# Optimization experiments

Hardware: AMD Instinct MI355X
Metric: run time of the kernel (lower is better)

The kernel has to match this reference:

```python
import jax, jax.numpy as jnp
import numpy as np

# ---- model constants (match init_kwargs) ----
NX, NY, H, K, GRID = 32, 1, 64, 3, 5
MID = 2 * H + 1            # 129, middle width of each KAN block
NB = GRID + K              # 8 B-spline basis functions per edge
BATCH = 65536


def _grid_pts():
    # uniform extended grid on [-1, 1] with K extra knots each side: GRID+2K+1 pts
    step = 2.0 / GRID
    return jnp.arange(-K, GRID + K + 1, dtype=jnp.float32) * step - 1.0


def bspline_basis(x):
    """Cox-de Boor B-spline bases. x: [B, I] -> [B, I, GRID+K]."""
    g = _grid_pts()[None, None, :]          # [1,1,P]
    xe = x[..., None]                       # [B,I,1]
    B0 = ((xe >= g[..., :-1]) & (xe < g[..., 1:])).astype(x.dtype)
    Bp = B0
    for p in range(1, K + 1):
        left = (xe - g[..., :-(p + 1)]) / (g[..., p:-1] - g[..., :-(p + 1)])
        right = (g[..., p + 1:] - xe) / (g[..., p + 1:] - g[..., 1:-p])
        Bp = left * Bp[..., :-1] + right * Bp[..., 1:]
    return Bp  # [B, I, NB]


def kan_layer(x, coef, sb, ss, bias):
    """pykan KANLayer: y_o = sum_i sb[i,o]*silu(x_i) + ss[i,o]*spline_io(x_i) + bias_o.
    x: [B,I]; coef: [I,O,NB]; sb, ss: [I,O]; bias: [O]."""
    bs = bspline_basis(x)                                   # [B,I,NB]
    spline = jnp.einsum('bip,iop->bo', bs, coef * ss[:, :, None])
    return jax.nn.silu(x) @ sb + spline + bias


def setup_inputs() -> dict:
    key = jax.random.key(0)
    ks = iter(jax.random.split(key, 40))

    def xavier(k, shape, fan_in, fan_out):
        gain = np.sqrt(2.0)  # relu gain, as in the torch module
        std = gain * np.sqrt(2.0 / (fan_in + fan_out))
        return (std * jax.random.normal(k, shape, dtype=jnp.float32))

    inp = {
        'x': jax.random.normal(next(ks), (BATCH, NX), dtype=jnp.float32),
        'W_in': xavier(next(ks), (NX, H), NX, H),
        'b_in': jnp.zeros((H,), jnp.float32),
        'W_out': xavier(next(ks), (H, NY), H, NY),
    }
    for l in range(2):  # num_hidden_layers KAN blocks, each = 2 KANLayers
        for tag, (din, dout) in [('a', (H, MID)), ('b', (MID, H))]:
            inp[f'coef{l}{tag}'] = xavier(next(ks), (din, dout, NB), din * NB, dout)
            inp[f'sb{l}{tag}'] = xavier(next(ks), (din, dout), din, dout)
            inp[f'ss{l}{tag}'] = jnp.ones((din, dout), jnp.float32)
            inp[f'bias{l}{tag}'] = jnp.zeros((dout,), jnp.float32)
    return inp


def reference(x, W_in, b_in, W_out,
              coef0a, sb0a, ss0a, bias0a, coef0b, sb0b, ss0b, bias0b,
              coef1a, sb1a, ss1a, bias1a, coef1b, sb1b, ss1b, bias1b):
    h = jax.nn.relu(x @ W_in + b_in)
    for (ca, sa, ta, ba, cb, sbb, tb, bb) in (
        (coef0a, sb0a, ss0a, bias0a, coef0b, sb0b, ss0b, bias0b),
        (coef1a, sb1a, ss1a, bias1a, coef1b, sb1b, ss1b, bias1b),
    ):
        h = kan_layer(h, ca, sa, ta, ba)   # H -> 2H+1
        h = kan_layer(h, cb, sbb, tb, bb)  # 2H+1 -> H
    return jax.nn.sigmoid(h @ W_out)       # [B, NY]
```

## Files before the change

kernel.cpp:

```cpp
#include <hip/hip_runtime.h>
#include <math.h>
#include <stdint.h>

#define BATCH 65536
#define TB 64

typedef __fp16   fp16x2 __attribute__((ext_vector_type(2)));
typedef _Float16 half8  __attribute__((ext_vector_type(8)));
typedef float   floatx4 __attribute__((ext_vector_type(4)));

#define SH 68
#define SM 130
#define HM_SLICE (16*SM + 64)

#define WIN 2048
#define KSA 18
#define KSB 39
#define WA (KSA*9*512)
#define WB (KSB*4*512)
#define WTOT (WIN + 2*(WA+WB))

__global__ void setup_weights(
    const float* __restrict__ W_in,
    const float* __restrict__ c0a, const float* __restrict__ sb0a, const float* __restrict__ ss0a,
    const float* __restrict__ c0b, const float* __restrict__ sb0b, const float* __restrict__ ss0b,
    const float* __restrict__ c1a, const float* __restrict__ sb1a, const float* __restrict__ ss1a,
    const float* __restrict__ c1b, const float* __restrict__ sb1b, const float* __restrict__ ss1b,
    _Float16* __restrict__ wt) {
  int idx = blockIdx.x * 256 + threadIdx.x;
  if (idx >= WTOT) return;
  float v = 0.0f;
  if (idx < WIN) {
    int nt = idx >> 9; int r = idx & 511; int l = r >> 3; int j = r & 7;
    int n = nt*16 + (l & 15);
    int k = (l >> 4)*8 + j;
    v = W_in[k*64 + n];
  } else {
    int e2   = idx - WIN;
    int pair = (e2 >= WA + WB) ? 1 : 0;
    int e    = e2 - pair * (WA + WB);
    if (e < WA) {
      const float* coef = pair ? c1a : c0a;
      const float* sb   = pair ? sb1a : sb0a;
      const float* ss   = pair ? ss1a : ss0a;
      int ks = e / 4608; int r = e - ks*4608;
      int nt = r >> 9;   int q = r & 511;
      int l  = q >> 3;   int j = q & 7;
      int n  = nt*16 + (l & 15);
      int k  = ks*32 + (l >> 4)*8 + j;
      if (n < 129) {
        if (k < 512) { int i = k >> 3, p = k & 7; v = ss[i*129+n] * coef[(i*129+n)*8 + p]; }
        else         { int i = k - 512;           v = sb[i*129+n]; }
      }
    } else {
      const float* coef = pair ? c1b : c0b;
      const float* sb   = pair ? sb1b : sb0b;
      const float* ss   = pair ? ss1b : ss0b;
      int eb = e - WA;
      int ks = eb >> 11; int r = eb & 2047;
      int nt = r >> 9;   int q = r & 511;
      int l  = q >> 3;   int j = q & 7;
      int n  = nt*16 + (l & 15);
      int k  = ks*32 + (l >> 4)*8 + j;
      if (k < 1088) { int i = k >> 3, p = k & 7; if (i < 129) v = ss[i*64+n] * coef[(i*64+n)*8 + p]; }
      else          { int i = k - 1088;          if (i < 129) v = sb[i*64+n]; }
    }
  }
  wt[idx] = (_Float16)v;
}

__device__ __forceinline__ half8 feat8(float x) {
  float s  = (x + 2.2f) * 2.5f;
  float mf = floorf(s);
  int   m  = (int)mf;
  float u  = s - mf;
  float t  = 1.0f - u;
  float u2 = u*u;
  float w0 = t*t*t * (1.0f/6.0f);
  float w3 = u2*u * (1.0f/6.0f);
  float w1 = fmaf(u2, fmaf(0.5f, u, -1.0f), 2.0f/3.0f);
  float w2 = 1.0f - w0 - w1 - w3;
  union { fp16x2 h2[2]; uint64_t u64; } P;
  P.h2[0] = __builtin_amdgcn_cvt_pkrtz(w0, w1);
  P.h2[1] = __builtin_amdgcn_cvt_pkrtz(w2, w3);
  uint64_t w01 = (m >= 0 && m <= 10) ? P.u64 : 0ull;
  int sh = (m - 3) * 16;
  uint64_t q0 = (sh >= 0) ? ((sh < 64) ? (w01 << sh) : 0ull) : (w01 >> (-sh));
  uint64_t q1 = (sh >= 64) ? (w01 << (sh - 64))
                           : ((sh > 0) ? (w01 >> (64 - sh)) : 0ull);
  union { uint64_t q[2]; half8 h; } R;
  R.q[0] = q0; R.q[1] = q1;
  return R.h;
}

template<int KSPL, int KSIL, int NT, int SIN, int O, int SOUT>
__device__ __forceinline__ void kan_layer(
    const _Float16* __restrict__ hinw, _Float16* __restrict__ houtw,
    const _Float16* __restrict__ wt, const float* __restrict__ bias, int lane) {
  constexpr int KTOT = KSPL + KSIL;
  constexpr int PF   = (NT > 4) ? 4 : NT;
  const int ln = lane & 15;
  const int kq = lane >> 4;
  const half8* __restrict__ bp = (const half8*)wt + lane;
  floatx4 acc[NT];
  #pragma unroll
  for (int j = 0; j < NT; ++j) acc[j] = (floatx4){0.f, 0.f, 0.f, 0.f};

  half8 Bpre[PF];
  #pragma unroll
  for (int j = 0; j < PF; ++j) Bpre[j] = bp[j*64];

  #pragma unroll 2
  for (int ks = 0; ks < KTOT; ++ks) {
    half8 A;
    if (ks < KSPL) {
      float xv = (float)hinw[ln*SIN + ks*4 + kq];
      A = feat8(xv);
    } else {
      int sk = ks - KSPL;
      half8 h8 = *(const half8*)&hinw[ln*SIN + sk*32 + kq*8];
      union { fp16x2 h2[4]; half8 v; } Au;
      #pragma unroll
      for (int e = 0; e < 4; ++e) {
        float x0 = (float)h8[2*e], x1 = (float)h8[2*e + 1];
        float s0 = x0 / (1.0f + __expf(-x0));
        float s1 = x1 / (1.0f + __expf(-x1));
        Au.h2[e] = __builtin_amdgcn_cvt_pkrtz(s0, s1);
      }
      A = Au.v;
    }
    half8 Bcur[PF];
    #pragma unroll
    for (int j = 0; j < PF; ++j) Bcur[j] = Bpre[j];
    const int nks = (ks + 1 < KTOT) ? (ks + 1) : ks;
    #pragma unroll
    for (int j = 0; j < PF; ++j) Bpre[j] = bp[(nks*NT + j)*64];
    #pragma unroll
    for (int j = 0; j < PF; ++j)
      acc[j] = __builtin_amdgcn_mfma_f32_16x16x32_f16(A, Bcur[j], acc[j], 0, 0, 0);
    #pragma unroll
    for (int j = PF; j < NT; ++j) {
      half8 B = bp[(ks*NT + j)*64];
      acc[j] = __builtin_amdgcn_mfma_f32_16x16x32_f16(A, B, acc[j], 0, 0, 0);
    }
  }

  #pragma unroll
  for (int j = 0; j < NT; ++j) {
    int col = j*16 + ln;
    if (col < O) {
      float bv = bias[col];
      #pragma unroll
      for (int r = 0; r < 4; ++r)
        houtw[(kq*4 + r)*SOUT + col] = (_Float16)(acc[j][r] + bv);
    }
  }
}

extern "C" __global__ void __launch_bounds__(256, 4)
kan_forward(const float* __restrict__ x, const float* __restrict__ b_in,
            const float* __restrict__ W_out, const _Float16* __restrict__ wt,
            const float* __restrict__ bias0a, const float* __restrict__ bias0b,
            const float* __restrict__ bias1a, const float* __restrict__ bias1b,
            float* __restrict__ out) {
  __shared__ _Float16 hM[4][HM_SLICE];
  __shared__ _Float16 hH[4][16*SH];
  const int t    = threadIdx.x;
  const int wv   = t >> 6;
  const int lane = t & 63;
  const int ln   = lane & 15;
  const int kq   = lane >> 4;
  _Float16* hMw = hM[wv];
  _Float16* hHw = hH[wv];
  const int rbase = blockIdx.x * TB + wv * 16;

  hMw[16*SM + lane] = (_Float16)0.0f;
  if (lane < 16) hMw[lane*SM + 129] = (_Float16)0.0f;

  {
    const float* xr = &x[(rbase + ln)*32 + kq*8];
    float4 v0 = *(const float4*)&xr[0];
    float4 v1 = *(const float4*)&xr[4];
    union { fp16x2 h2[4]; half8 h8; } A;
    A.h2[0] = __builtin_amdgcn_cvt_pkrtz(v0.x, v0.y);
    A.h2[1] = __builtin_amdgcn_cvt_pkrtz(v0.z, v0.w);
    A.h2[2] = __builtin_amdgcn_cvt_pkrtz(v1.x, v1.y);
    A.h2[3] = __builtin_amdgcn_cvt_pkrtz(v1.z, v1.w);
    const half8* bp = (const half8*)wt + lane;
    #pragma unroll
    for (int nt = 0; nt < 4; ++nt) {
      floatx4 z = (floatx4){0.f, 0.f, 0.f, 0.f};
      half8 B = bp[nt*64];
      floatx4 a = __builtin_amdgcn_mfma_f32_16x16x32_f16(A.h8, B, z, 0, 0, 0);
      int col = nt*16 + ln;
      float bv = b_in[col];
      #pragma unroll
      for (int r = 0; r < 4; ++r)
        hHw[(kq*4 + r)*SH + col] = (_Float16)fmaxf(a[r] + bv, 0.0f);
    }
  }

  kan_layer<16,2,9,SH,129,SM>(hHw, hMw, wt + WIN,             bias0a, lane);
  kan_layer<34,5,4,SM, 64,SH>(hMw, hHw, wt + WIN + WA,        bias0b, lane);
  kan_layer<16,2,9,SH,129,SM>(hHw, hMw, wt + WIN + WA + WB,   bias1a, lane);
  kan_layer<34,5,4,SM, 64,SH>(hMw, hHw, wt + WIN + 2*WA + WB, bias1b, lane);

  {
    float s = 0.0f;
    #pragma unroll
    for (int j = 0; j < 16; ++j)
      s = fmaf((float)hHw[ln*SH + kq*16 + j], W_out[kq*16 + j], s);
    s += __shfl_down(s, 32);
    s += __shfl_down(s, 16);
    if (lane < 16) out[rbase + ln] = 1.0f / (1.0f + __expf(-s));
  }
}

extern "C" void kernel_launch(void* const* d_in, const int* in_sizes, int n_in,
                              void* d_out, int out_size, void* d_ws, size_t ws_size,
                              hipStream_t stream) {
  const float* x     = (const float*)d_in[0];
  const float* W_in  = (const float*)d_in[1];
  const float* b_in  = (const float*)d_in[2];
  const float* W_out = (const float*)d_in[3];
  const float* c0a = (const float*)d_in[4];  const float* sb0a = (const float*)d_in[5];
  const float* ss0a= (const float*)d_in[6];  const float* bias0a=(const float*)d_in[7];
  const float* c0b = (const float*)d_in[8];  const float* sb0b = (const float*)d_in[9];
  const float* ss0b= (const float*)d_in[10]; const float* bias0b=(const float*)d_in[11];
  const float* c1a = (const float*)d_in[12]; const float* sb1a = (const float*)d_in[13];
  const float* ss1a= (const float*)d_in[14]; const float* bias1a=(const float*)d_in[15];
  const float* c1b = (const float*)d_in[16]; const float* sb1b = (const float*)d_in[17];
  const float* ss1b= (const float*)d_in[18]; const float* bias1b=(const float*)d_in[19];
  float*    out = (float*)d_out;
  _Float16* wt  = (_Float16*)d_ws;

  setup_weights<<<(WTOT + 255)/256, 256, 0, stream>>>(
      W_in, c0a, sb0a, ss0a, c0b, sb0b, ss0b,
      c1a, sb1a, ss1a, c1b, sb1b, ss1b, wt);

  kan_forward<<<BATCH/TB, 256, 0, stream>>>(
      x, b_in, W_out, wt, bias0a, bias0b, bias1a, bias1b, out);
}
```

Before: 176.7 us.

## Switch KAN layers to 32x32x16 MFMA with 32-row wave tiles

Each wave now handles 32 batch rows and uses the 32x32x16 f16 MFMA instead of 16x16x32. The packed weight layout is rebuilt for the new tile shape, and the B-operand prefetch becomes a two-stage full-width double buffer. The aim is to reuse each weight fragment across twice as many rows and cut weight-load traffic per row. In exchange, accumulators and shared memory per wave grow and occupancy is lowered to 2 blocks per SM. The layer-b spline K range is also tightened from 1088 to 1040, which removes some padded k-steps.

```diff
diff --git a/kernel.cpp b/kernel.cpp
--- a/kernel.cpp
+++ b/kernel.cpp
@@ -3,21 +3,21 @@
 #include <stdint.h>
 
 #define BATCH 65536
-#define TB 64
-
-typedef __fp16   fp16x2 __attribute__((ext_vector_type(2)));
-typedef _Float16 half8  __attribute__((ext_vector_type(8)));
-typedef float   floatx4 __attribute__((ext_vector_type(4)));
+#define TB 128
+
+typedef __fp16   fp16x2  __attribute__((ext_vector_type(2)));
+typedef _Float16 half8   __attribute__((ext_vector_type(8)));
+typedef float    floatx16 __attribute__((ext_vector_type(16)));
 
 #define SH 68
 #define SM 130
-#define HM_SLICE (16*SM + 64)
+#define HM_SLICE (32*SM + 64)
 
 #define WIN 2048
-#define KSA 18
-#define KSB 39
-#define WA (KSA*9*512)
-#define WB (KSB*4*512)
+#define KSA 36
+#define KSB 74
+#define WA (KSA*5*512)
+#define WB (KSB*2*512)
 #define WTOT (WIN + 2*(WA+WB))
 
 __global__ void setup_weights(
@@ -31,9 +31,10 @@
   if (idx >= WTOT) return;
   float v = 0.0f;
   if (idx < WIN) {
-    int nt = idx >> 9; int r = idx & 511; int l = r >> 3; int j = r & 7;
-    int n = nt*16 + (l & 15);
-    int k = (l >> 4)*8 + j;
+    int ks = idx >> 10; int nt = (idx >> 9) & 1;
+    int q = idx & 511;  int l = q >> 3;   int j = q & 7;
+    int n = nt*32 + (l & 31);
+    int k = ks*16 + (l >> 5)*8 + j;
     v = W_in[k*64 + n];
   } else {
     int e2   = idx - WIN;
@@ -43,11 +44,11 @@
       const float* coef = pair ? c1a : c0a;
       const float* sb   = pair ? sb1a : sb0a;
       const float* ss   = pair ? ss1a : ss0a;
-      int ks = e / 4608; int r = e - ks*4608;
+      int ks = e / 2560; int r = e - ks*2560;
       int nt = r >> 9;   int q = r & 511;
       int l  = q >> 3;   int j = q & 7;
-      int n  = nt*16 + (l & 15);
-      int k  = ks*32 + (l >> 4)*8 + j;
+      int n  = nt*32 + (l & 31);
+      int k  = ks*16 + (l >> 5)*8 + j;
       if (n < 129) {
         if (k < 512) { int i = k >> 3, p = k & 7; v = ss[i*129+n] * coef[(i*129+n)*8 + p]; }
         else         { int i = k - 512;           v = sb[i*129+n]; }
@@ -57,13 +58,13 @@
       const float* sb   = pair ? sb1b : sb0b;
       const float* ss   = pair ? ss1b : ss0b;
       int eb = e - WA;
-      int ks = eb >> 11; int r = eb & 2047;
+      int ks = eb >> 10; int r = eb & 1023;
       int nt = r >> 9;   int q = r & 511;
       int l  = q >> 3;   int j = q & 7;
-      int n  = nt*16 + (l & 15);
-      int k  = ks*32 + (l >> 4)*8 + j;
-      if (k < 1088) { int i = k >> 3, p = k & 7; if (i < 129) v = ss[i*64+n] * coef[(i*64+n)*8 + p]; }
-      else          { int i = k - 1088;          if (i < 129) v = sb[i*64+n]; }
+      int n  = nt*32 + (l & 31);
+      int k  = ks*16 + (l >> 5)*8 + j;
+      if (k < 1032)      { int i = k >> 3, p = k & 7; v = ss[i*64+n] * coef[(i*64+n)*8 + p]; }
+      else if (k >= 1040){ int s = k - 1040; if (s < 129) v = sb[s*64+n]; }
     }
   }
   wt[idx] = (_Float16)v;
@@ -98,27 +99,30 @@
     const _Float16* __restrict__ hinw, _Float16* __restrict__ houtw,
     const _Float16* __restrict__ wt, const float* __restrict__ bias, int lane) {
   constexpr int KTOT = KSPL + KSIL;
-  constexpr int PF   = (NT > 4) ? 4 : NT;
-  const int ln = lane & 15;
-  const int kq = lane >> 4;
+  const int ln = lane & 31;
+  const int kh = lane >> 5;
   const half8* __restrict__ bp = (const half8*)wt + lane;
-  floatx4 acc[NT];
-  #pragma unroll
-  for (int j = 0; j < NT; ++j) acc[j] = (floatx4){0.f, 0.f, 0.f, 0.f};
-
-  half8 Bpre[PF];
-  #pragma unroll
-  for (int j = 0; j < PF; ++j) Bpre[j] = bp[j*64];
+  floatx16 acc[NT];
+  #pragma unroll
+  for (int j = 0; j < NT; ++j)
+    #pragma unroll
+    for (int e = 0; e < 16; ++e) acc[j][e] = 0.0f;
+
+  half8 B0[NT], B1[NT];
+  #pragma unroll
+  for (int j = 0; j < NT; ++j) B0[j] = bp[j*64];
+  #pragma unroll
+  for (int j = 0; j < NT; ++j) B1[j] = bp[(NT + j)*64];
 
   #pragma unroll 2
   for (int ks = 0; ks < KTOT; ++ks) {
     half8 A;
     if (ks < KSPL) {
-      float xv = (float)hinw[ln*SIN + ks*4 + kq];
+      float xv = (float)hinw[ln*SIN + 2*ks + kh];
       A = feat8(xv);
     } else {
       int sk = ks - KSPL;
-      half8 h8 = *(const half8*)&hinw[ln*SIN + sk*32 + kq*8];
+      half8 h8 = *(const half8*)&hinw[ln*SIN + sk*16 + kh*8];
       union { fp16x2 h2[4]; half8 v; } Au;
       #pragma unroll
       for (int e = 0; e < 4; ++e) {
@@ -129,90 +133,96 @@
       }
       A = Au.v;
     }
-    half8 Bcur[PF];
-    #pragma unroll
-    for (int j = 0; j < PF; ++j) Bcur[j] = Bpre[j];
-    const int nks = (ks + 1 < KTOT) ? (ks + 1) : ks;
-    #pragma unroll
-    for (int j = 0; j < PF; ++j) Bpre[j] = bp[(nks*NT + j)*64];
-    #pragma unroll
-    for (int j = 0; j < PF; ++j)
-      acc[j] = __builtin_amdgcn_mfma_f32_16x16x32_f16(A, Bcur[j], acc[j], 0, 0, 0);
-    #pragma unroll
-    for (int j = PF; j < NT; ++j) {
-      half8 B = bp[(ks*NT + j)*64];
-      acc[j] = __builtin_amdgcn_mfma_f32_16x16x32_f16(A, B, acc[j], 0, 0, 0);
-    }
+    half8 Bcur[NT];
+    #pragma unroll
+    for (int j = 0; j < NT; ++j) { Bcur[j] = B0[j]; B0[j] = B1[j]; }
+    const int nks = (ks + 2 < KTOT) ? (ks + 2) : (KTOT - 1);
+    #pragma unroll
+    for (int j = 0; j < NT; ++j) B1[j] = bp[(nks*NT + j)*64];
+    #pragma unroll
+    for (int j = 0; j < NT; ++j)
+      acc[j] = __builtin_amdgcn_mfma_f32_32x32x16_f16(A, Bcur[j], acc[j], 0, 0, 0);
   }
 
   #pragma unroll
   for (int j = 0; j < NT; ++j) {
-    int col = j*16 + ln;
+    int col = j*32 + ln;
     if (col < O) {
       float bv = bias[col];
       #pragma unroll
-      for (int r = 0; r < 4; ++r)
-        houtw[(kq*4 + r)*SOUT + col] = (_Float16)(acc[j][r] + bv);
-    }
-  }
-}
-
-extern "C" __global__ void __launch_bounds__(256, 4)
+      for (int r = 0; r < 16; ++r) {
+        int row = (r & 3) + 8*(r >> 2) + 4*kh;
+        houtw[row*SOUT + col] = (_Float16)(acc[j][r] + bv);
+      }
+    }
+  }
+}
+
+extern "C" __global__ void __launch_bounds__(256, 2)
 kan_forward(const float* __restrict__ x, const float* __restrict__ b_in,
             const float* __restrict__ W_out, const _Float16* __restrict__ wt,
             const float* __restrict__ bias0a, const float* __restrict__ bias0b,
             const float* __restrict__ bias1a, const float* __restrict__ bias1b,
             float* __restrict__ out) {
   __shared__ _Float16 hM[4][HM_SLICE];
-  __shared__ _Float16 hH[4][16*SH];
+  __shared__ _Float16 hH[4][32*SH];
   const int t    = threadIdx.x;
   const int wv   = t >> 6;
   const int lane = t & 63;
-  const int ln   = lane & 15;
-  const int kq   = lane >> 4;
+  const int ln   = lane & 31;
+  const int kh   = lane >> 5;
   _Float16* hMw = hM[wv];
   _Float16* hHw = hH[wv];
-  const int rbase = blockIdx.x * TB + wv * 16;
-
-  hMw[16*SM + lane] = (_Float16)0.0f;
-  if (lane < 16) hMw[lane*SM + 129] = (_Float16)0.0f;
+  const int rbase = blockIdx.x * TB + wv * 32;
+
+  hMw[32*SM + lane] = (_Float16)0.0f;
+  if (lane < 32) hMw[lane*SM + 129] = (_Float16)0.0f;
 
   {
-    const float* xr = &x[(rbase + ln)*32 + kq*8];
+    const float* xr = &x[(rbase + ln)*32 + kh*8];
     float4 v0 = *(const float4*)&xr[0];
     float4 v1 = *(const float4*)&xr[4];
-    union { fp16x2 h2[4]; half8 h8; } A;
-    A.h2[0] = __builtin_amdgcn_cvt_pkrtz(v0.x, v0.y);
-    A.h2[1] = __builtin_amdgcn_cvt_pkrtz(v0.z, v0.w);
-    A.h2[2] = __builtin_amdgcn_cvt_pkrtz(v1.x, v1.y);
-    A.h2[3] = __builtin_amdgcn_cvt_pkrtz(v1.z, v1.w);
+    float4 v2 = *(const float4*)&xr[16];
+    float4 v3 = *(const float4*)&xr[20];
+    union { fp16x2 h2[4]; half8 h8; } A0, A1;
+    A0.h2[0] = __builtin_amdgcn_cvt_pkrtz(v0.x, v0.y);
+    A0.h2[1] = __builtin_amdgcn_cvt_pkrtz(v0.z, v0.w);
+    A0.h2[2] = __builtin_amdgcn_cvt_pkrtz(v1.x, v1.y);
+    A0.h2[3] = __builtin_amdgcn_cvt_pkrtz(v1.z, v1.w);
+    A1.h2[0] = __builtin_amdgcn_cvt_pkrtz(v2.x, v2.y);
+    A1.h2[1] = __builtin_amdgcn_cvt_pkrtz(v2.z, v2.w);
+    A1.h2[2] = __builtin_amdgcn_cvt_pkrtz(v3.x, v3.y);
+    A1.h2[3] = __builtin_amdgcn_cvt_pkrtz(v3.z, v3.w);
     const half8* bp = (const half8*)wt + lane;
     #pragma unroll
-    for (int nt = 0; nt < 4; ++nt) {
-      floatx4 z = (floatx4){0.f, 0.f, 0.f, 0.f};
-      half8 B = bp[nt*64];
-      floatx4 a = __builtin_amdgcn_mfma_f32_16x16x32_f16(A.h8, B, z, 0, 0, 0);
-      int col = nt*16 + ln;
+    for (int nt = 0; nt < 2; ++nt) {
+      floatx16 a;
+      #pragma unroll
+      for (int e = 0; e < 16; ++e) a[e] = 0.0f;
+      a = __builtin_amdgcn_mfma_f32_32x32x16_f16(A0.h8, bp[nt*64],       a, 0, 0, 0);
+      a = __builtin_amdgcn_mfma_f32_32x32x16_f16(A1.h8, bp[(2 + nt)*64], a, 0, 0, 0);
+      int col = nt*32 + ln;
       float bv = b_in[col];
       #pragma unroll
-      for (int r = 0; r < 4; ++r)
-        hHw[(kq*4 + r)*SH + col] = (_Float16)fmaxf(a[r] + bv, 0.0f);
-    }
-  }
-
-  kan_layer<16,2,9,SH,129,SM>(hHw, hMw, wt + WIN,             bias0a, lane);
-  kan_layer<34,5,4,SM, 64,SH>(hMw, hHw, wt + WIN + WA,        bias0b, lane);
-  kan_layer<16,2,9,SH,129,SM>(hHw, hMw, wt + WIN + WA + WB,   bias1a, lane);
-  kan_layer<34,5,4,SM, 64,SH>(hMw, hHw, wt + WIN + 2*WA + WB, bias1b, lane);
+      for (int r = 0; r < 16; ++r) {
+        int row = (r & 3) + 8*(r >> 2) + 4*kh;
+        hHw[row*SH + col] = (_Float16)fmaxf(a[r] + bv, 0.0f);
+      }
+    }
+  }
+
+  kan_layer<32,4,5,SH,129,SM>(hHw, hMw, wt + WIN,             bias0a, lane);
+  kan_layer<65,9,2,SM, 64,SH>(hMw, hHw, wt + WIN + WA,        bias0b, lane);
+  kan_layer<32,4,5,SH,129,SM>(hHw, hMw, wt + WIN + WA + WB,   bias1a, lane);
+  kan_layer<65,9,2,SM, 64,SH>(hMw, hHw, wt + WIN + 2*WA + WB, bias1b, lane);
 
   {
     float s = 0.0f;
     #pragma unroll
-    for (int j = 0; j < 16; ++j)
-      s = fmaf((float)hHw[ln*SH + kq*16 + j], W_out[kq*16 + j], s);
+    for (int j = 0; j < 32; ++j)
+      s = fmaf((float)hHw[ln*SH + kh*32 + j], W_out[kh*32 + j], s);
     s += __shfl_down(s, 32);
-    s += __shfl_down(s, 16);
-    if (lane < 16) out[rbase + ln] = 1.0f / (1.0f + __expf(-s));
+    if (lane < 32) out[rbase + ln] = 1.0f / (1.0f + __expf(-s));
   }
 }
 
```

New measurement: 170.1 us. 1.04x faster.
